# Performance work log

Hardware: AMD Instinct MI355X
Metric: run time of the kernel (lower is better)

## Reference

```python
import jax, jax.numpy as jnp
import numpy as np

NEG_INF = -1e9
NEG_SLOPE = 0.2


def setup_inputs() -> dict:
    key = jax.random.key(0)
    k1, k2, k3, k4, k5 = jax.random.split(key, 5)
    N, in_dim, out_dim = 8192, 256, 128
    x = jax.random.normal(k1, (N, in_dim), dtype=jnp.float32)
    adj = jax.random.randint(k2, (N, N), 0, 2, dtype=jnp.int32)
    # xavier_uniform for W (stored as [in_dim, out_dim] so h = x @ W)
    limit = float(np.sqrt(6.0 / (in_dim + out_dim)))
    W = jax.random.uniform(k3, (in_dim, out_dim), minval=-limit, maxval=limit, dtype=jnp.float32)
    a_src = 0.1 * jax.random.normal(k4, (out_dim,), dtype=jnp.float32)
    a_dst = 0.1 * jax.random.normal(k5, (out_dim,), dtype=jnp.float32)
    return {"x": x, "adj": adj, "W": W, "a_src": a_src, "a_dst": a_dst}


def reference(x, adj, W, a_src, a_dst):
    # h: [N, out_dim]
    h = x @ W
    src = h @ a_src  # [N]
    dst = h @ a_dst  # [N]
    e = jax.nn.leaky_relu(src[:, None] + dst[None, :], negative_slope=NEG_SLOPE)
    e = jnp.where(adj > 0, e, NEG_INF)
    alpha = jax.nn.softmax(e, axis=1)  # row-wise softmax over neighbors
    # dropout is identity in eval mode (reference uses training=False)
    return alpha @ h
```

## Files before the change

### kernel.cpp

```cpp
#include <hip/hip_runtime.h>
#include <hip/hip_bf16.h>

typedef __attribute__((ext_vector_type(8))) short bf16x8;
typedef __attribute__((ext_vector_type(4))) float f32x4;
typedef __attribute__((ext_vector_type(16))) float f32x16;

#define N_NODES 8192
#define D_IN    256
#define D_OUT   128
#define LOG2E   1.44269504088896f

__device__ __forceinline__ unsigned short bf16_rne(float f) {
  unsigned int u = __float_as_uint(f);
  u += 0x7fffu + ((u >> 16) & 1u);
  return (unsigned short)(u >> 16);
}
__device__ __forceinline__ float bf16_to_f(unsigned short s) {
  return __uint_as_float(((unsigned int)s) << 16);
}
__device__ __forceinline__ unsigned int pack_bf16x2(float lo, float hi) {
  __hip_bfloat162 b2 = __float22bfloat162_rn(make_float2(lo, hi));
  union { __hip_bfloat162 b; unsigned int u; } cv;
  cv.b = b2;
  return cv.u;
}

__global__ __launch_bounds__(256) void k_split_x(const float* __restrict__ x,
                                                 unsigned short* __restrict__ xhi,
                                                 unsigned short* __restrict__ xlo) {
  int idx = (blockIdx.x * 256 + threadIdx.x) * 8;
  float4 v0 = *(const float4*)(x + idx);
  float4 v1 = *(const float4*)(x + idx + 4);
  float v[8] = {v0.x, v0.y, v0.z, v0.w, v1.x, v1.y, v1.z, v1.w};
  unsigned int hw[4], lw[4];
#pragma unroll
  for (int p = 0; p < 4; ++p) {
    unsigned short h0 = bf16_rne(v[2 * p]);
    unsigned short h1 = bf16_rne(v[2 * p + 1]);
    unsigned short l0 = bf16_rne(v[2 * p] - bf16_to_f(h0));
    unsigned short l1 = bf16_rne(v[2 * p + 1] - bf16_to_f(h1));
    hw[p] = (unsigned int)h0 | ((unsigned int)h1 << 16);
    lw[p] = (unsigned int)l0 | ((unsigned int)l1 << 16);
  }
  *(uint4*)(xhi + idx) = make_uint4(hw[0], hw[1], hw[2], hw[3]);
  *(uint4*)(xlo + idx) = make_uint4(lw[0], lw[1], lw[2], lw[3]);
}

__global__ __launch_bounds__(256) void k_split_w(const float* __restrict__ W,
                                                 unsigned short* __restrict__ whiT,
                                                 unsigned short* __restrict__ wloT) {
  int c = blockIdx.x;
  int k = threadIdx.x;
  float v = W[k * D_OUT + c];
  unsigned short h = bf16_rne(v);
  unsigned short l = bf16_rne(v - bf16_to_f(h));
  whiT[c * D_IN + k] = h;
  wloT[c * D_IN + k] = l;
}

__global__ __launch_bounds__(256) void k_h_gemm(const unsigned short* __restrict__ xhi,
                                                const unsigned short* __restrict__ xlo,
                                                const unsigned short* __restrict__ whiT,
                                                const unsigned short* __restrict__ wloT,
                                                const float* __restrict__ a_src,
                                                const float* __restrict__ a_dst,
                                                float* __restrict__ srcv,
                                                float* __restrict__ dstv,
                                                unsigned short* __restrict__ phi) {
  __shared__ float h_s[32][128];
  const int t = threadIdx.x, l = t & 63, wv = t >> 6;
  const int i0 = blockIdx.x * 32;
  const int m = wv >> 1, nh = wv & 1;
  const int frow = l & 15, kq = l >> 4;
  const size_t arow = (size_t)(i0 + m * 16 + frow);
  const unsigned short* pah = xhi + arow * D_IN + kq * 8;
  const unsigned short* pal = xlo + arow * D_IN + kq * 8;
  f32x4 acc[4];
#pragma unroll
  for (int nf = 0; nf < 4; ++nf) acc[nf] = (f32x4){0.f, 0.f, 0.f, 0.f};
#pragma unroll
  for (int kk = 0; kk < 8; ++kk) {
    const int k0 = kk * 32;
    bf16x8 ah = *(const bf16x8*)(pah + k0);
    bf16x8 al = *(const bf16x8*)(pal + k0);
#pragma unroll
    for (int nf = 0; nf < 4; ++nf) {
      const int col = nh * 64 + nf * 16 + frow;
      bf16x8 bh = *(const bf16x8*)(whiT + (size_t)col * D_IN + k0 + kq * 8);
      bf16x8 bl = *(const bf16x8*)(wloT + (size_t)col * D_IN + k0 + kq * 8);
      acc[nf] = __builtin_amdgcn_mfma_f32_16x16x32_bf16(ah, bh, acc[nf], 0, 0, 0);
      acc[nf] = __builtin_amdgcn_mfma_f32_16x16x32_bf16(al, bh, acc[nf], 0, 0, 0);
      acc[nf] = __builtin_amdgcn_mfma_f32_16x16x32_bf16(ah, bl, acc[nf], 0, 0, 0);
    }
  }
#pragma unroll
  for (int nf = 0; nf < 4; ++nf)
#pragma unroll
    for (int r = 0; r < 4; ++r)
      h_s[m * 16 + kq * 4 + r][nh * 64 + nf * 16 + frow] = acc[nf][r];
  __syncthreads();

  if (t < 32) {
    float s = 0.f, d = 0.f;
#pragma unroll
    for (int c = 0; c < D_OUT; ++c) {
      float v = h_s[t][c];
      s += v * a_src[c];
      d += v * a_dst[c];
    }
    srcv[i0 + t] = s * LOG2E;
    dstv[i0 + t] = d * LOG2E;
  }

  {
    const int b = t >> 7, ct = (t >> 5) & 3, lw = t & 31;
    const size_t kg = (size_t)(i0 / 16 + b);
#pragma unroll
    for (int half = 0; half < 2; ++half) {
      const int lane = lw + 32 * half;
      unsigned int hw[4];
#pragma unroll
      for (int p = 0; p < 4; ++p) {
        float v0 = h_s[b * 16 + half * 8 + 2 * p][ct * 32 + lw];
        float v1 = h_s[b * 16 + half * 8 + 2 * p + 1][ct * 32 + lw];
        hw[p] = (unsigned int)bf16_rne(v0) | ((unsigned int)bf16_rne(v1) << 16);
      }
      const size_t off = ((kg * 4 + ct) * 64 + lane) * 8;
      *(uint4*)(phi + off) = make_uint4(hw[0], hw[1], hw[2], hw[3]);
    }
  }
}

__global__ __launch_bounds__(1024) void k_gat(const int* __restrict__ adj,
                                              const float* __restrict__ srcv,
                                              const float* __restrict__ dstv,
                                              const unsigned short* __restrict__ phi,
                                              float* __restrict__ out) {
  __shared__ unsigned long long mbuf[2][8][33];
  __shared__ float dstv_s[8192];
  __shared__ float red[2][2048];
  __shared__ float rsl[8][32];

  const int t = threadIdx.x, l = t & 63, wv = t >> 6;
  const int ch = wv >> 3, js = wv & 7;
  const int i0 = blockIdx.x * 32;
  const int r32 = l & 31, kh = l >> 5;

  ((float4*)dstv_s)[t] = ((const float4*)dstv)[t];
  ((float4*)dstv_s)[t + 1024] = ((const float4*)dstv)[t + 1024];
  const float s2 = srcv[i0 + r32];

  const int* abase = adj + (size_t)(i0 + 2 * wv) * N_NODES + l;

  int cva[16];
#pragma unroll
  for (int s = 0; s < 16; ++s)
    cva[s] = __builtin_nontemporal_load(abase + (s >> 3) * N_NODES + (s & 7) * 64);
#pragma unroll
  for (int s = 0; s < 16; ++s) {
    unsigned long long b = __ballot(cva[s] > 0);
    if (l == 0) mbuf[0][s & 7][2 * wv + (s >> 3)] = b;
  }
#pragma unroll
  for (int s = 0; s < 16; ++s)
    cva[s] = __builtin_nontemporal_load(abase + (s >> 3) * N_NODES + 512 + (s & 7) * 64);

  const unsigned short* pb0 = phi + ((size_t)((js * 2) * 4 + ch * 2) * 64 + l) * 8;
  bf16x8 b00A = *(const bf16x8*)(pb0);
  bf16x8 b01A = *(const bf16x8*)(pb0 + 512);
  bf16x8 b10A = *(const bf16x8*)(pb0 + 2048);
  bf16x8 b11A = *(const bf16x8*)(pb0 + 2048 + 512);

  const int shl = (js & 1) * 32 + kh * 8;
  const int w0 = js >> 1;

  f32x16 acc0, acc1;
#pragma unroll
  for (int q = 0; q < 16; ++q) { acc0[q] = 0.f; acc1[q] = 0.f; }
  float rs = 0.f;

  __syncthreads();

  for (int c = 0; c < 16; ++c) {
#pragma unroll
    for (int it = 0; it < 2; ++it) {
      int nc = c, nit = it + 1;
      if (nit == 2) { nit = 0; nc = (c < 15) ? c + 1 : 15; }
      const unsigned short* pan = pb0 + nc * 65536 + nit * 32768;
      bf16x8 b00B = *(const bf16x8*)(pan);
      bf16x8 b01B = *(const bf16x8*)(pan + 512);
      bf16x8 b10B = *(const bf16x8*)(pan + 2048);
      bf16x8 b11B = *(const bf16x8*)(pan + 2048 + 512);
      __builtin_amdgcn_sched_barrier(0);

      const unsigned long long mw = mbuf[c & 1][it * 4 + w0][r32];
      const int jl = c * 512 + it * 256 + js * 32 + kh * 8;
      const unsigned int u0 = (unsigned int)(mw >> shl) & 0xFFu;
      const unsigned int u1 = (unsigned int)(mw >> (shl + 16)) & 0xFFu;

#pragma unroll
      for (int ks = 0; ks < 2; ++ks) {
        f32x4 dva = *(const f32x4*)&dstv_s[jl + ks * 16];
        f32x4 dvb = *(const f32x4*)&dstv_s[jl + ks * 16 + 4];
        const unsigned int u = ks ? u1 : u0;
        float w[8];
#pragma unroll
        for (int e = 0; e < 4; ++e) {
          float e0 = s2 + dva[e]; e0 = fmaxf(e0, 0.2f * e0);
          float e1 = s2 + dvb[e]; e1 = fmaxf(e1, 0.2f * e1);
          w[e]     = ((u >> e) & 1u)       ? exp2f(e0) : 0.f;
          w[4 + e] = ((u >> (4 + e)) & 1u) ? exp2f(e1) : 0.f;
        }
        if (ch == 0)
          rs += ((w[0] + w[1]) + (w[2] + w[3])) + ((w[4] + w[5]) + (w[6] + w[7]));
        union { bf16x8 v; unsigned int u4[4]; } af;
#pragma unroll
        for (int p = 0; p < 4; ++p)
          af.u4[p] = pack_bf16x2(w[2 * p], w[2 * p + 1]);

        if (ks == 0) {
          acc0 = __builtin_amdgcn_mfma_f32_32x32x16_bf16(af.v, b00A, acc0, 0, 0, 0);
          acc1 = __builtin_amdgcn_mfma_f32_32x32x16_bf16(af.v, b01A, acc1, 0, 0, 0);
        } else {
          acc0 = __builtin_amdgcn_mfma_f32_32x32x16_bf16(af.v, b10A, acc0, 0, 0, 0);
          acc1 = __builtin_amdgcn_mfma_f32_32x32x16_bf16(af.v, b11A, acc1, 0, 0, 0);
        }
      }
      b00A = b00B; b01A = b01B; b10A = b10B; b11A = b11B;
    }

    if (c < 15) {
#pragma unroll
      for (int s = 0; s < 16; ++s) {
        unsigned long long b = __ballot(cva[s] > 0);
        if (l == 0) mbuf[(c + 1) & 1][s & 7][2 * wv + (s >> 3)] = b;
      }
      if (c < 14) {
        const int nb = (c + 2) * 512;
#pragma unroll
        for (int s = 0; s < 16; ++s)
          cva[s] = __builtin_nontemporal_load(abase + (s >> 3) * N_NODES + nb + (s & 7) * 64);
      }
    }
    __syncthreads();
  }

  rs += __shfl_xor(rs, 32);
  if (ch == 0 && kh == 0) rsl[js][r32] = rs;

#pragma unroll
  for (int q = 1; q < 8; ++q) {
    if (js == q) {
#pragma unroll
      for (int reg = 0; reg < 16; ++reg) {
        red[ch][reg * 64 + l] = acc0[reg];
        red[ch][1024 + reg * 64 + l] = acc1[reg];
      }
    }
    __syncthreads();
    if (js == 0) {
#pragma unroll
      for (int reg = 0; reg < 16; ++reg) {
        acc0[reg] += red[ch][reg * 64 + l];
        acc1[reg] += red[ch][1024 + reg * 64 + l];
      }
    }
    __syncthreads();
  }

  if (js == 0) {
#pragma unroll
    for (int reg = 0; reg < 16; ++reg) {
      const int row = (reg & 3) + 8 * (reg >> 2) + 4 * kh;
      const float rsum = (((rsl[0][row] + rsl[1][row]) + (rsl[2][row] + rsl[3][row])) +
                          ((rsl[4][row] + rsl[5][row]) + (rsl[6][row] + rsl[7][row])));
      out[(size_t)(i0 + row) * D_OUT + ch * 64 + r32] = acc0[reg] / rsum;
      out[(size_t)(i0 + row) * D_OUT + ch * 64 + 32 + r32] = acc1[reg] / rsum;
    }
  }
}

extern "C" void kernel_launch(void* const* d_in, const int* in_sizes, int n_in,
                              void* d_out, int out_size, void* d_ws, size_t ws_size,
                              hipStream_t stream) {
  const float* x     = (const float*)d_in[0];
  const int*   adj   = (const int*)d_in[1];
  const float* W     = (const float*)d_in[2];
  const float* a_src = (const float*)d_in[3];
  const float* a_dst = (const float*)d_in[4];
  float* out = (float*)d_out;

  char* ws = (char*)d_ws;
  unsigned short* xhi  = (unsigned short*)(ws);
  unsigned short* xlo  = (unsigned short*)(ws + (4 << 20));
  unsigned short* whiT = (unsigned short*)(ws + (8 << 20));
  unsigned short* wloT = (unsigned short*)(ws + (8 << 20) + (64 << 10));
  unsigned short* phi  = (unsigned short*)(ws + (8 << 20) + (128 << 10));
  float*          srcv = (float*)(ws + (12 << 20) + (128 << 10));
  float*          dstv = (float*)(ws + (12 << 20) + (160 << 10));

  k_split_x<<<dim3(1024), dim3(256), 0, stream>>>(x, xhi, xlo);
  k_split_w<<<dim3(128), dim3(256), 0, stream>>>(W, whiT, wloT);
  k_h_gemm<<<dim3(256), dim3(256), 0, stream>>>(xhi, xlo, whiT, wloT,
                                                a_src, a_dst, srcv, dstv, phi);
  k_gat<<<dim3(256), dim3(1024), 0, stream>>>(adj, srcv, dstv, phi, out);
}
```

Baseline: 112.3 us.

## Fuse x split into GEMM and split GAT columns across two blocks per tile

The separate kernel that splits x into bf16 hi/lo parts is removed, and that conversion now happens inline inside the h GEMM as x is loaded in fp32. The GAT kernel now splits the neighbor dimension in two halves, using 512 blocks of 512 threads instead of 256 blocks of 1024, to raise occupancy and spread the adjacency stream over more CUs. Each half writes its partial numerators and row sums to workspace, and a new combine kernel adds the two halves and normalizes. This adds an extra launch and about 8 MB of partial-sum traffic in exchange for the added parallelism.

```diff
diff --git a/kernel.cpp b/kernel.cpp
--- a/kernel.cpp
+++ b/kernel.cpp
@@ -23,27 +23,6 @@
   union { __hip_bfloat162 b; unsigned int u; } cv;
   cv.b = b2;
   return cv.u;
-}
-
-__global__ __launch_bounds__(256) void k_split_x(const float* __restrict__ x,
-                                                 unsigned short* __restrict__ xhi,
-                                                 unsigned short* __restrict__ xlo) {
-  int idx = (blockIdx.x * 256 + threadIdx.x) * 8;
-  float4 v0 = *(const float4*)(x + idx);
-  float4 v1 = *(const float4*)(x + idx + 4);
-  float v[8] = {v0.x, v0.y, v0.z, v0.w, v1.x, v1.y, v1.z, v1.w};
-  unsigned int hw[4], lw[4];
-#pragma unroll
-  for (int p = 0; p < 4; ++p) {
-    unsigned short h0 = bf16_rne(v[2 * p]);
-    unsigned short h1 = bf16_rne(v[2 * p + 1]);
-    unsigned short l0 = bf16_rne(v[2 * p] - bf16_to_f(h0));
-    unsigned short l1 = bf16_rne(v[2 * p + 1] - bf16_to_f(h1));
-    hw[p] = (unsigned int)h0 | ((unsigned int)h1 << 16);
-    lw[p] = (unsigned int)l0 | ((unsigned int)l1 << 16);
-  }
-  *(uint4*)(xhi + idx) = make_uint4(hw[0], hw[1], hw[2], hw[3]);
-  *(uint4*)(xlo + idx) = make_uint4(lw[0], lw[1], lw[2], lw[3]);
 }
 
 __global__ __launch_bounds__(256) void k_split_w(const float* __restrict__ W,
@@ -58,8 +37,7 @@
   wloT[c * D_IN + k] = l;
 }
 
-__global__ __launch_bounds__(256) void k_h_gemm(const unsigned short* __restrict__ xhi,
-                                                const unsigned short* __restrict__ xlo,
+__global__ __launch_bounds__(256) void k_h_gemm(const float* __restrict__ x,
                                                 const unsigned short* __restrict__ whiT,
                                                 const unsigned short* __restrict__ wloT,
                                                 const float* __restrict__ a_src,
@@ -73,24 +51,30 @@
   const int m = wv >> 1, nh = wv & 1;
   const int frow = l & 15, kq = l >> 4;
   const size_t arow = (size_t)(i0 + m * 16 + frow);
-  const unsigned short* pah = xhi + arow * D_IN + kq * 8;
-  const unsigned short* pal = xlo + arow * D_IN + kq * 8;
+  const float* px = x + arow * D_IN + kq * 8;
   f32x4 acc[4];
 #pragma unroll
   for (int nf = 0; nf < 4; ++nf) acc[nf] = (f32x4){0.f, 0.f, 0.f, 0.f};
 #pragma unroll
   for (int kk = 0; kk < 8; ++kk) {
     const int k0 = kk * 32;
-    bf16x8 ah = *(const bf16x8*)(pah + k0);
-    bf16x8 al = *(const bf16x8*)(pal + k0);
+    float4 xv0 = *(const float4*)(px + k0);
+    float4 xv1 = *(const float4*)(px + k0 + 4);
+    float xv[8] = {xv0.x, xv0.y, xv0.z, xv0.w, xv1.x, xv1.y, xv1.z, xv1.w};
+    union { bf16x8 v; unsigned short s[8]; } ah, al;
+#pragma unroll
+    for (int e = 0; e < 8; ++e) {
+      ah.s[e] = bf16_rne(xv[e]);
+      al.s[e] = bf16_rne(xv[e] - bf16_to_f(ah.s[e]));
+    }
 #pragma unroll
     for (int nf = 0; nf < 4; ++nf) {
       const int col = nh * 64 + nf * 16 + frow;
       bf16x8 bh = *(const bf16x8*)(whiT + (size_t)col * D_IN + k0 + kq * 8);
       bf16x8 bl = *(const bf16x8*)(wloT + (size_t)col * D_IN + k0 + kq * 8);
-      acc[nf] = __builtin_amdgcn_mfma_f32_16x16x32_bf16(ah, bh, acc[nf], 0, 0, 0);
-      acc[nf] = __builtin_amdgcn_mfma_f32_16x16x32_bf16(al, bh, acc[nf], 0, 0, 0);
-      acc[nf] = __builtin_amdgcn_mfma_f32_16x16x32_bf16(ah, bl, acc[nf], 0, 0, 0);
+      acc[nf] = __builtin_amdgcn_mfma_f32_16x16x32_bf16(ah.v, bh, acc[nf], 0, 0, 0);
+      acc[nf] = __builtin_amdgcn_mfma_f32_16x16x32_bf16(al.v, bh, acc[nf], 0, 0, 0);
+      acc[nf] = __builtin_amdgcn_mfma_f32_16x16x32_bf16(ah.v, bl, acc[nf], 0, 0, 0);
     }
   }
 #pragma unroll
@@ -131,41 +115,45 @@
   }
 }
 
-__global__ __launch_bounds__(1024) void k_gat(const int* __restrict__ adj,
-                                              const float* __restrict__ srcv,
-                                              const float* __restrict__ dstv,
-                                              const unsigned short* __restrict__ phi,
-                                              float* __restrict__ out) {
-  __shared__ unsigned long long mbuf[2][8][33];
-  __shared__ float dstv_s[8192];
+__global__ __launch_bounds__(512, 4) void k_gat(const int* __restrict__ adj,
+                                                const float* __restrict__ srcv,
+                                                const float* __restrict__ dstv,
+                                                const unsigned short* __restrict__ phi,
+                                                float* __restrict__ pnum,
+                                                float* __restrict__ prsum) {
+  __shared__ unsigned long long mbuf[2][4][33];
+  __shared__ float dstv_s[4096];
   __shared__ float red[2][2048];
-  __shared__ float rsl[8][32];
+  __shared__ float rsl[4][32];
 
   const int t = threadIdx.x, l = t & 63, wv = t >> 6;
-  const int ch = wv >> 3, js = wv & 7;
-  const int i0 = blockIdx.x * 32;
+  const int ch = wv >> 2, js = wv & 3;
+  const int bid = blockIdx.x;
+  const int tile = bid & 255, jh = bid >> 8;
+  const int i0 = tile * 32;
   const int r32 = l & 31, kh = l >> 5;
 
-  ((float4*)dstv_s)[t] = ((const float4*)dstv)[t];
-  ((float4*)dstv_s)[t + 1024] = ((const float4*)dstv)[t + 1024];
+  ((float4*)dstv_s)[t] = ((const float4*)(dstv + jh * 4096))[t];
+  ((float4*)dstv_s)[t + 512] = ((const float4*)(dstv + jh * 4096))[t + 512];
   const float s2 = srcv[i0 + r32];
 
-  const int* abase = adj + (size_t)(i0 + 2 * wv) * N_NODES + l;
+  const int* abase = adj + (size_t)(i0 + 4 * wv) * N_NODES + jh * 4096 + l;
 
   int cva[16];
 #pragma unroll
   for (int s = 0; s < 16; ++s)
-    cva[s] = __builtin_nontemporal_load(abase + (s >> 3) * N_NODES + (s & 7) * 64);
+    cva[s] = __builtin_nontemporal_load(abase + (s >> 2) * N_NODES + (s & 3) * 64);
 #pragma unroll
   for (int s = 0; s < 16; ++s) {
     unsigned long long b = __ballot(cva[s] > 0);
-    if (l == 0) mbuf[0][s & 7][2 * wv + (s >> 3)] = b;
+    if (l == 0) mbuf[0][s & 3][4 * wv + (s >> 2)] = b;
   }
 #pragma unroll
   for (int s = 0; s < 16; ++s)
-    cva[s] = __builtin_nontemporal_load(abase + (s >> 3) * N_NODES + 512 + (s & 7) * 64);
-
-  const unsigned short* pb0 = phi + ((size_t)((js * 2) * 4 + ch * 2) * 64 + l) * 8;
+    cva[s] = __builtin_nontemporal_load(abase + (s >> 2) * N_NODES + 256 + (s & 3) * 64);
+
+  const int kst0 = jh * 256 + js * 2;
+  const unsigned short* pb0 = phi + ((size_t)(kst0 * 4 + ch * 2) * 64 + l) * 8;
   bf16x8 b00A = *(const bf16x8*)(pb0);
   bf16x8 b01A = *(const bf16x8*)(pb0 + 512);
   bf16x8 b10A = *(const bf16x8*)(pb0 + 2048);
@@ -186,15 +174,15 @@
     for (int it = 0; it < 2; ++it) {
       int nc = c, nit = it + 1;
       if (nit == 2) { nit = 0; nc = (c < 15) ? c + 1 : 15; }
-      const unsigned short* pan = pb0 + nc * 65536 + nit * 32768;
+      const unsigned short* pan = pb0 + nc * 32768 + nit * 16384;
       bf16x8 b00B = *(const bf16x8*)(pan);
       bf16x8 b01B = *(const bf16x8*)(pan + 512);
       bf16x8 b10B = *(const bf16x8*)(pan + 2048);
       bf16x8 b11B = *(const bf16x8*)(pan + 2048 + 512);
       __builtin_amdgcn_sched_barrier(0);
 
-      const unsigned long long mw = mbuf[c & 1][it * 4 + w0][r32];
-      const int jl = c * 512 + it * 256 + js * 32 + kh * 8;
+      const unsigned long long mw = mbuf[c & 1][it * 2 + w0][r32];
+      const int jl = c * 256 + it * 128 + js * 32 + kh * 8;
       const unsigned int u0 = (unsigned int)(mw >> shl) & 0xFFu;
       const unsigned int u1 = (unsigned int)(mw >> (shl + 16)) & 0xFFu;
 
@@ -233,13 +221,13 @@
 #pragma unroll
       for (int s = 0; s < 16; ++s) {
         unsigned long long b = __ballot(cva[s] > 0);
-        if (l == 0) mbuf[(c + 1) & 1][s & 7][2 * wv + (s >> 3)] = b;
+        if (l == 0) mbuf[(c + 1) & 1][s & 3][4 * wv + (s >> 2)] = b;
       }
       if (c < 14) {
-        const int nb = (c + 2) * 512;
+        const int nb = (c + 2) * 256;
 #pragma unroll
         for (int s = 0; s < 16; ++s)
-          cva[s] = __builtin_nontemporal_load(abase + (s >> 3) * N_NODES + nb + (s & 7) * 64);
+          cva[s] = __builtin_nontemporal_load(abase + (s >> 2) * N_NODES + nb + (s & 3) * 64);
       }
     }
     __syncthreads();
@@ -249,7 +237,7 @@
   if (ch == 0 && kh == 0) rsl[js][r32] = rs;
 
 #pragma unroll
-  for (int q = 1; q < 8; ++q) {
+  for (int q = 1; q < 4; ++q) {
     if (js == q) {
 #pragma unroll
       for (int reg = 0; reg < 16; ++reg) {
@@ -269,15 +257,32 @@
   }
 
   if (js == 0) {
+    float* pn = pnum + (size_t)bid * 4096;
 #pragma unroll
     for (int reg = 0; reg < 16; ++reg) {
       const int row = (reg & 3) + 8 * (reg >> 2) + 4 * kh;
-      const float rsum = (((rsl[0][row] + rsl[1][row]) + (rsl[2][row] + rsl[3][row])) +
-                          ((rsl[4][row] + rsl[5][row]) + (rsl[6][row] + rsl[7][row])));
-      out[(size_t)(i0 + row) * D_OUT + ch * 64 + r32] = acc0[reg] / rsum;
-      out[(size_t)(i0 + row) * D_OUT + ch * 64 + 32 + r32] = acc1[reg] / rsum;
-    }
-  }
+      pn[row * 128 + ch * 64 + r32] = acc0[reg];
+      pn[row * 128 + ch * 64 + 32 + r32] = acc1[reg];
+    }
+    if (ch == 0 && kh == 0)
+      prsum[bid * 32 + r32] = (rsl[0][r32] + rsl[1][r32]) + (rsl[2][r32] + rsl[3][r32]);
+  }
+}
+
+__global__ __launch_bounds__(1024) void k_comb(const float* __restrict__ pnum,
+                                               const float* __restrict__ prsum,
+                                               float* __restrict__ out) {
+  const int tile = blockIdx.x, t = threadIdx.x;
+  const float4 a = ((const float4*)(pnum + (size_t)tile * 4096))[t];
+  const float4 b = ((const float4*)(pnum + (size_t)(256 + tile) * 4096))[t];
+  const int row = t >> 5;
+  const float r = prsum[tile * 32 + row] + prsum[(256 + tile) * 32 + row];
+  float4 o;
+  o.x = (a.x + b.x) / r;
+  o.y = (a.y + b.y) / r;
+  o.z = (a.z + b.z) / r;
+  o.w = (a.w + b.w) / r;
+  ((float4*)(out + (size_t)tile * 4096))[t] = o;
 }
 
 extern "C" void kernel_launch(void* const* d_in, const int* in_sizes, int n_in,
@@ -291,17 +296,17 @@
   float* out = (float*)d_out;
 
   char* ws = (char*)d_ws;
-  unsigned short* xhi  = (unsigned short*)(ws);
-  unsigned short* xlo  = (unsigned short*)(ws + (4 << 20));
-  unsigned short* whiT = (unsigned short*)(ws + (8 << 20));
-  unsigned short* wloT = (unsigned short*)(ws + (8 << 20) + (64 << 10));
-  unsigned short* phi  = (unsigned short*)(ws + (8 << 20) + (128 << 10));
-  float*          srcv = (float*)(ws + (12 << 20) + (128 << 10));
-  float*          dstv = (float*)(ws + (12 << 20) + (160 << 10));
-
-  k_split_x<<<dim3(1024), dim3(256), 0, stream>>>(x, xhi, xlo);
+  float*          pnum = (float*)(ws);
+  float*          prsum= (float*)(ws + (8 << 20));
+  unsigned short* whiT = (unsigned short*)(ws + (8 << 20) + (64 << 10));
+  unsigned short* wloT = (unsigned short*)(ws + (8 << 20) + (128 << 10));
+  unsigned short* phi  = (unsigned short*)(ws + (8 << 20) + (192 << 10));
+  float*          srcv = (float*)(ws + (10 << 20) + (192 << 10));
+  float*          dstv = (float*)(ws + (10 << 20) + (224 << 10));
+
   k_split_w<<<dim3(128), dim3(256), 0, stream>>>(W, whiT, wloT);
-  k_h_gemm<<<dim3(256), dim3(256), 0, stream>>>(xhi, xlo, whiT, wloT,
+  k_h_gemm<<<dim3(256), dim3(256), 0, stream>>>(x, whiT, wloT,
                                                 a_src, a_dst, srcv, dstv, phi);
-  k_gat<<<dim3(256), dim3(1024), 0, stream>>>(adj, srcv, dstv, phi, out);
-}
+  k_gat<<<dim3(512), dim3(512), 0, stream>>>(adj, srcv, dstv, phi, pnum, prsum);
+  k_comb<<<dim3(256), dim3(1024), 0, stream>>>(pnum, prsum, out);
+}
```

Result: faster. 110.0 us (-2.0%).
